# Kernel optimization log

Measured on AMD Instinct MI355X. Metric: run time of the kernel, lower is better.

The kernel has to match this reference:

```python
import jax, jax.numpy as jnp
from jax import lax
import numpy as np

WINDOW_SIZES = (1, 2, 3)


def _proj(x, w1, b1, w2, b2):
    # gated projection: sigmoid(Linear1) * tanh(Linear2)
    return jax.nn.sigmoid(x @ w1.T + b1) * jnp.tanh(x @ w2.T + b2)


def setup_inputs() -> dict:
    key = jax.random.key(0)
    ks = jax.random.split(key, 16)
    V, E, D = 50000, 1024, 1024
    N, La, Lq = 64, 512, 64
    s = 0.02  # weight scale to keep sigmoid/tanh unsaturated
    return {
        "data_q": jax.random.randint(ks[0], (Lq,), 0, V),
        "data_as": jax.random.randint(ks[1], (N, La), 0, V),
        "emb": jax.random.normal(ks[2], (V, E), jnp.float32),
        "w1": jax.random.normal(ks[3], (D, E), jnp.float32) * s,
        "b1": jnp.zeros((D,), jnp.float32),
        "w2": jax.random.normal(ks[4], (D, E), jnp.float32) * s,
        "b2": jnp.zeros((D,), jnp.float32),
        "cw1": jax.random.normal(ks[5], (D, D, 1), jnp.float32) * s,
        "cb1": jnp.zeros((D,), jnp.float32),
        "cw2": jax.random.normal(ks[6], (D, D, 2), jnp.float32) * s,
        "cb2": jnp.zeros((D,), jnp.float32),
        "cw3": jax.random.normal(ks[7], (D, D, 3), jnp.float32) * s,
        "cb3": jnp.zeros((D,), jnp.float32),
        "lin_w": jax.random.normal(ks[8], (D, 3 * D), jnp.float32) * s,
        "lin_b": jnp.zeros((D,), jnp.float32),
        "soft_w": jax.random.normal(ks[9], (1, D), jnp.float32) * s,
        "soft_b": jnp.zeros((1,), jnp.float32),
    }


def reference(data_q, data_as, emb, w1, b1, w2, b2,
              cw1, cb1, cw2, cb2, cw3, cb3, lin_w, lin_b, soft_w, soft_b):
    N, La = data_as.shape
    a_tok = data_as.reshape(-1)                     # [T] concatenated answers
    emb_a = emb[a_tok]                              # [T, E]
    emb_q = emb[data_q]                             # [Lq, E]
    pa = _proj(emb_a, w1, b1, w2, b2)               # [T, D]
    pq = _proj(emb_q, w1, b1, w2, b2)               # [Lq, D]

    # attention: M_r = q @ a^T ; alpha = softmax over question positions
    M = pq @ pa.T                                   # [Lq, T]
    alpha = jax.nn.softmax(M.T, axis=1)             # [T, Lq]
    Y = alpha @ pq                                  # [T, D]
    sim = pa * Y                                    # elementwise compare (mul)

    starts = jnp.arange(N) * La
    x = sim.T[None]                                 # [1, D, T]
    pools = []
    for w, cw, cb in zip(WINDOW_SIZES, (cw1, cw2, cw3), (cb1, cb2, cb3)):
        conv = lax.conv_general_dilated(
            x, cw, (1,), 'VALID',
            dimension_numbers=('NCW', 'OIW', 'NCW'))[0].T + cb  # [T-w+1, D]
        conv = jax.nn.relu(conv)
        # DMax: per-answer max over rows [start_k, start_k + La - w + 1)
        idx = starts[:, None] + jnp.arange(La - w + 1)[None, :]  # [N, La-w+1]
        pools.append(conv[idx].max(axis=1))          # [N, D]

    cat = jnp.concatenate(pools, axis=1)            # [N, 3D]
    h = jnp.tanh(cat @ lin_w.T + lin_b)             # [N, D]
    logits = (h @ soft_w.T + soft_b).reshape(-1)    # [N]
    return jax.nn.log_softmax(logits)
```

## Files before the change

kernel.cpp:

```cpp
#include <hip/hip_runtime.h>

#define DEV __device__ __forceinline__

typedef __bf16 bf16x8 __attribute__((ext_vector_type(8)));
typedef float f32x4 __attribute__((ext_vector_type(4)));
typedef unsigned short u16;
typedef u16 u16x4 __attribute__((ext_vector_type(4)));

constexpr int T_ANS = 32768;
constexpr int LQ    = 64;
constexpr int M_ALL = T_ANS + LQ;
constexpr int M_PAD = 33024;
constexpr int DIM   = 1024;

DEV u16 f2bf(float x) {
  unsigned u = __float_as_uint(x);
  return (u16)((u + 0x7FFFu + ((u >> 16) & 1u)) >> 16);
}
DEV float bf2f(u16 s) { return __uint_as_float(((unsigned)s) << 16); }

DEV void gl2lds16(const void* g, void* l) {
  __builtin_amdgcn_global_load_lds(
      (const __attribute__((address_space(1))) unsigned int*)g,
      (__attribute__((address_space(3))) unsigned int*)l, 16, 0, 0);
}

#define MF(A, B, C) __builtin_amdgcn_mfma_f32_16x16x32_bf16(A, B, C, 0, 0, 0)
#define LFC(P, OFF) (*(const bf16x8*)((P) + (OFF)))


#define STG(G, LT, R0) gl2lds16((G) + (R0) * 2048 + gOff, (LT) + (R0) * 64 + ldOff)

#define S_TILE(AT, BT, BUF)                                                           \
  { const char* ga_ = (AT); const char* gb_ = (BT); char* lb_ = (BUF);                \
    STG(ga_, lb_, 0); STG(ga_, lb_, 128);                                             \
    STG(gb_, lb_ + 16384, 0); STG(gb_, lb_ + 16384, 128); }

#define VMC4 asm volatile("s_waitcnt vmcnt(4)" ::: "memory");
#define VMC0 asm volatile("s_waitcnt vmcnt(0)" ::: "memory");

#define TILEV3(BUF, STAGES, WAIT)                                                     \
  {                                                                                   \
    STAGES                                                                            \
    const char* Ar = (BUF) + rdA;                                                     \
    const char* Br = (BUF) + 16384 + rdB;                                             \
    bf16x8 a0 = LFC(Ar, 0),    a1 = LFC(Ar, 1024), a2 = LFC(Ar, 2048), a3 = LFC(Ar, 3072); \
    bf16x8 a4 = LFC(Ar, 4096), a5 = LFC(Ar, 5120), a6 = LFC(Ar, 6144), a7 = LFC(Ar, 7168); \
    bf16x8 c0 = LFC(Br, 0), c1 = LFC(Br, 1024), c2 = LFC(Br, 2048), c3 = LFC(Br, 3072);    \
    acc[0][0] = MF(a0, c0, acc[0][0]); acc[0][1] = MF(a0, c1, acc[0][1]);             \
    acc[0][2] = MF(a0, c2, acc[0][2]); acc[0][3] = MF(a0, c3, acc[0][3]);             \
    acc[1][0] = MF(a1, c0, acc[1][0]); acc[1][1] = MF(a1, c1, acc[1][1]);             \
    acc[1][2] = MF(a1, c2, acc[1][2]); acc[1][3] = MF(a1, c3, acc[1][3]);             \
    acc[2][0] = MF(a2, c0, acc[2][0]); acc[2][1] = MF(a2, c1, acc[2][1]);             \
    acc[2][2] = MF(a2, c2, acc[2][2]); acc[2][3] = MF(a2, c3, acc[2][3]);             \
    acc[3][0] = MF(a3, c0, acc[3][0]); acc[3][1] = MF(a3, c1, acc[3][1]);             \
    acc[3][2] = MF(a3, c2, acc[3][2]); acc[3][3] = MF(a3, c3, acc[3][3]);             \
    acc[4][0] = MF(a4, c0, acc[4][0]); acc[4][1] = MF(a4, c1, acc[4][1]);             \
    acc[4][2] = MF(a4, c2, acc[4][2]); acc[4][3] = MF(a4, c3, acc[4][3]);             \
    acc[5][0] = MF(a5, c0, acc[5][0]); acc[5][1] = MF(a5, c1, acc[5][1]);             \
    acc[5][2] = MF(a5, c2, acc[5][2]); acc[5][3] = MF(a5, c3, acc[5][3]);             \
    acc[6][0] = MF(a6, c0, acc[6][0]); acc[6][1] = MF(a6, c1, acc[6][1]);             \
    acc[6][2] = MF(a6, c2, acc[6][2]); acc[6][3] = MF(a6, c3, acc[6][3]);             \
    acc[7][0] = MF(a7, c0, acc[7][0]); acc[7][1] = MF(a7, c1, acc[7][1]);             \
    acc[7][2] = MF(a7, c2, acc[7][2]); acc[7][3] = MF(a7, c3, acc[7][3]);             \
    WAIT                                                                              \
    asm volatile("s_barrier" ::: "memory");                                           \
  }

#define GEMM_V3(NT)                                                                   \
  f32x4 acc[8][4] = {};                                                               \
  const int ldOff = tid * 16;                                                         \
  const int gOff = (tid >> 2) * 2048 + (((tid & 3) ^ ((tid >> 2) & 3)) << 4);         \
  const int blk_ = (((lane >> 4) ^ (lane & 3)) << 4);                                 \
  const int rdA = (wm + (lane & 15)) * 64 + blk_;                                     \
  const int rdB = (wn + (lane & 15)) * 64 + blk_;                                     \
  char* b0_ = lds; char* b1_ = lds + 32768; char* b2_ = lds + 65536; char* b3_ = lds + 98304; \
  S_TILE(Ab(0), Bb(0), b0_) S_TILE(Ab(1), Bb(1), b1_)                                 \
  VMC4                                                                                \
  asm volatile("s_barrier" ::: "memory");                                             \
  for (int g = 0; g < (NT) / 4 - 1; ++g) {                                            \
    const int t = 4 * g;                                                              \
    TILEV3(b0_, S_TILE(Ab(t + 2), Bb(t + 2), b2_), VMC4)                              \
    TILEV3(b1_, S_TILE(Ab(t + 3), Bb(t + 3), b3_), VMC4)                              \
    TILEV3(b2_, S_TILE(Ab(t + 4), Bb(t + 4), b0_), VMC4)                              \
    TILEV3(b3_, S_TILE(Ab(t + 5), Bb(t + 5), b1_), VMC4)                              \
  }                                                                                   \
  {                                                                                   \
    const int t = (NT) - 4;                                                           \
    TILEV3(b0_, S_TILE(Ab(t + 2), Bb(t + 2), b2_), VMC4)                              \
    TILEV3(b1_, S_TILE(Ab(t + 3), Bb(t + 3), b3_), VMC4)                              \
    TILEV3(b2_, , VMC0)                                                               \
    TILEV3(b3_, , )                                                                   \
  }


__global__ __launch_bounds__(256)
void prep_all(const float* __restrict__ w1, const float* __restrict__ w2,
              u16* __restrict__ W12,
              const float* __restrict__ lin_w, u16* __restrict__ linb,
              const float* __restrict__ cw1, const float* __restrict__ cw2,
              const float* __restrict__ cw3, u16* __restrict__ cwb,
              float* __restrict__ cat,
              const int* __restrict__ dq, const int* __restrict__ das,
              const float* __restrict__ emb, u16* __restrict__ X) {
  const int b = blockIdx.x, t = threadIdx.x;
  if (b < 8192) {
    int i = b * 256 + t;
    int n2 = i >> 10, k = i & 1023;
    int j = n2 >> 4, m = n2 & 15;
    const float* src = (j & 1) ? w2 : w1;
    W12[i] = f2bf(src[(size_t)((j >> 1) * 16 + m) * 1024 + k]);
  } else if (b < 11264) {
    int i = (b - 8192) * 256 + t;
    float4 v = ((const float4*)lin_w)[i];
    u16x4 o = { f2bf(v.x), f2bf(v.y), f2bf(v.z), f2bf(v.w) };
    ((u16x4*)linb)[i] = o;
  } else if (b < 23552) {
    int rb = b - 11264;
    int W = 1 + (rb >> 12);
    int i = (rb & 4095) * 256 + t;
    const float* src = (W == 1) ? cw1 : (W == 2) ? cw2 : cw3;
    u16* dst = cwb + ((W == 1) ? 0 : (W == 2) ? (size_t)1 * 1048576 : (size_t)3 * 1048576);
#pragma unroll 3
    for (int k = 0; k < 3; ++k)
      if (k < W)
        dst[(size_t)k * 1048576 + i] = f2bf(src[(size_t)i * W + k]);
  } else if (b < 24320) {
    cat[(b - 23552) * 256 + t] = 0.f;
  } else {
    const int row = b - 24320;
    size_t dsto = (size_t)row * DIM + t * 4;
    if (row >= M_ALL) {
      u16x4 z = {0, 0, 0, 0};
      *(u16x4*)(X + dsto) = z;
      return;
    }
    const int tok = (row < T_ANS) ? das[row] : dq[row - T_ANS];
    float4 v = ((const float4*)(emb + (size_t)tok * DIM))[t];
    u16x4 o = { f2bf(v.x), f2bf(v.y), f2bf(v.z), f2bf(v.w) };
    *(u16x4*)(X + dsto) = o;
  }
}

__global__ void transpose_pq(const u16* __restrict__ pa, u16* __restrict__ pqT) {
  int i = blockIdx.x * 256 + threadIdx.x;
  int e = i >> 6, q = i & 63;
  pqT[i] = pa[(size_t)(T_ANS + q) * DIM + e];
}

__global__ void zero_pad_sim(u16* __restrict__ sim) {
  int i = blockIdx.x * 256 + threadIdx.x;
  if (i < 2 * DIM) sim[(size_t)T_ANS * DIM + i] = 0;
}

__global__ void cast_cat(const float* __restrict__ cat, u16* __restrict__ catb) {
  int i = blockIdx.x * 256 + threadIdx.x;
  if (i < 128 * 3072) {
    int row = i / 3072;
    catb[i] = (row < 64) ? f2bf(cat[i]) : (u16)0;
  }
}


__global__ __launch_bounds__(256)
void proj_g(const u16* __restrict__ X, const u16* __restrict__ W12,
            const float* __restrict__ b1, const float* __restrict__ b2,
            u16* __restrict__ pa) {
  __shared__ alignas(16) u16 sA[128 * 32];
  __shared__ alignas(16) u16 sB[128 * 32];
  const int tid = threadIdx.x, lane = tid & 63;
  const int wid = tid >> 6;
  const int wm = (wid >> 1) * 64, wn = (wid & 1) * 64;
  const int wg = ((int)blockIdx.x % 8) * 516 + (int)blockIdx.x / 8;
  const int tm = (wg >> 4) * 128, tn = (wg & 15) * 128;
  f32x4 acc[4][4] = {};
  for (int k0 = 0; k0 < 1024; k0 += 32) {
#pragma unroll
    for (int j = 0; j < 2; ++j) {
      const int f = tid * 16 + j * 4096;
      const int r = f >> 6, cb = f & 63;
      gl2lds16((const char*)X   + (size_t)(tm + r) * 2048 + k0 * 2 + cb, (char*)sA + f);
      gl2lds16((const char*)W12 + (size_t)(tn + r) * 2048 + k0 * 2 + cb, (char*)sB + f);
    }
    __syncthreads();
    const int lr = lane & 15, lk = (lane >> 4) * 8;
    bf16x8 af[4], bf[4];
#pragma unroll
    for (int i = 0; i < 4; ++i) {
      af[i] = *(const bf16x8*)(sA + (wm + i * 16 + lr) * 32 + lk);
      bf[i] = *(const bf16x8*)(sB + (wn + i * 16 + lr) * 32 + lk);
    }
#pragma unroll
    for (int mi = 0; mi < 4; ++mi)
#pragma unroll
      for (int ni = 0; ni < 4; ++ni)
        acc[mi][ni] = MF(af[mi], bf[ni], acc[mi][ni]);
    __syncthreads();
  }
  const int lr = lane & 15, lg = (lane >> 4) * 4;
#pragma unroll
  for (int np = 0; np < 2; ++np) {
    const int col = ((tn + wn) >> 1) + np * 16 + lr;
    const float b1v = b1[col], b2v = b2[col];
#pragma unroll
    for (int mi = 0; mi < 4; ++mi)
#pragma unroll
      for (int r = 0; r < 4; ++r) {
        const int row = tm + wm + mi * 16 + lg + r;
        const float x1 = acc[mi][2 * np][r] + b1v;
        const float x2 = acc[mi][2 * np + 1][r] + b2v;
        const float sg = 1.f / (1.f + __expf(-x1));
        const float th = 2.f / (1.f + __expf(-2.f * x2)) - 1.f;
        pa[(size_t)row * DIM + col] = f2bf(sg * th);
      }
  }
}


template<int W>
__global__ __launch_bounds__(512, 1)
void conv_g(const u16* __restrict__ sim, const u16* __restrict__ Bw,
            const float* __restrict__ cb, float* __restrict__ cat) {
  extern __shared__ char lds[];
  const int tid = threadIdx.x, lane = tid & 63;
  const int wid = tid >> 6;
  const int wm = (wid >> 2) * 128, wn = (wid & 3) * 64;
  const int lr = lane & 15;
  const int wg = ((int)blockIdx.x % 8) * 64 + (int)blockIdx.x / 8;
  const int tm = (wg >> 2) * 256, tn = (wg & 3) * 256;
  const char* Ag = (const char*)sim + (size_t)tm * 2048;
  const char* Bg = (const char*)Bw + (size_t)tn * 2048;
  auto Ab = [&](int t) { return Ag + (t >> 5) * 2048 + ((t & 31) << 6); };
  auto Bb = [&](int t) { return Bg + (size_t)(t >> 5) * 2097152 + ((t & 31) << 6); };

  GEMM_V3(32 * W)

  const int lg = (lane >> 4) * 4;
  const int n = tm >> 9;
#pragma unroll
  for (int ni = 0; ni < 4; ++ni) {
    const int col = tn + wn + ni * 16 + lr;
    const float cbv = cb[col];
    float vmax = 0.f;
#pragma unroll
    for (int mi = 0; mi < 8; ++mi)
#pragma unroll
      for (int r = 0; r < 4; ++r) {
        const int t = tm + wm + mi * 16 + lg + r;
        float v = fmaxf(acc[mi][ni][r] + cbv, 0.f);
        if ((t & 511) > 512 - W) v = 0.f;
        vmax = fmaxf(vmax, v);
      }
    vmax = fmaxf(vmax, __shfl_xor(vmax, 16));
    vmax = fmaxf(vmax, __shfl_xor(vmax, 32));
    if (lane < 16)
      atomicMax((int*)&cat[(size_t)n * 3072 + (W - 1) * 1024 + col], __float_as_int(vmax));
  }
}


__global__ __launch_bounds__(256, 2)
void attn_s(const u16* __restrict__ pa, float* __restrict__ Spart) {
  __shared__ alignas(16) u16 sA[128 * 32];
  __shared__ alignas(16) u16 sB[64 * 32];
  const int tid = threadIdx.x, lane = tid & 63;
  const int tm = blockIdx.x * 128;
  const int kbase = blockIdx.y * 256;
  const int wid = tid >> 6;
  const int wm = (wid >> 1) * 64, wn = (wid & 1) * 32;
  const u16* pq = pa + (size_t)T_ANS * DIM;
  f32x4 acc[4][2] = {};
  for (int k0 = kbase; k0 < kbase + 256; k0 += 32) {
#pragma unroll
    for (int j = 0; j < 2; ++j) {
      const int f = tid * 16 + j * 4096;
      const int r = f >> 6, cb = f & 63;
      gl2lds16((const char*)pa + (size_t)(tm + r) * 2048 + k0 * 2 + cb, (char*)sA + f);
    }
    {
      const int f = tid * 16;
      const int r = f >> 6, cb = f & 63;
      gl2lds16((const char*)pq + (size_t)r * 2048 + k0 * 2 + cb, (char*)sB + f);
    }
    __syncthreads();
    const int lr = lane & 15, lk = (lane >> 4) * 8;
    bf16x8 af[4], bfr[2];
#pragma unroll
    for (int i = 0; i < 4; ++i)
      af[i] = *(const bf16x8*)(sA + (wm + i * 16 + lr) * 32 + lk);
#pragma unroll
    for (int i = 0; i < 2; ++i)
      bfr[i] = *(const bf16x8*)(sB + (wn + i * 16 + lr) * 32 + lk);
#pragma unroll
    for (int mi = 0; mi < 4; ++mi)
#pragma unroll
      for (int ni = 0; ni < 2; ++ni)
        acc[mi][ni] = MF(af[mi], bfr[ni], acc[mi][ni]);
    __syncthreads();
  }
  const int lr = lane & 15, lg = (lane >> 4) * 4;
  float* Sp = Spart + (size_t)blockIdx.y * (T_ANS * 64);
#pragma unroll
  for (int mi = 0; mi < 4; ++mi)
#pragma unroll
    for (int ni = 0; ni < 2; ++ni)
#pragma unroll
      for (int r = 0; r < 4; ++r) {
        const int row = tm + wm + mi * 16 + lg + r;
        const int col = wn + ni * 16 + lr;
        Sp[(size_t)row * 64 + col] = acc[mi][ni][r];
      }
}

__global__ void softmax64(const float* __restrict__ Spart, u16* __restrict__ alpha) {
  const int row = blockIdx.x * 4 + (threadIdx.x >> 6);
  const int lane = threadIdx.x & 63;
  const size_t o = (size_t)row * 64 + lane;
  float v = Spart[o] + Spart[(size_t)1 * T_ANS * 64 + o]
          + Spart[(size_t)2 * T_ANS * 64 + o] + Spart[(size_t)3 * T_ANS * 64 + o];
  float m = v;
#pragma unroll
  for (int o2 = 32; o2 > 0; o2 >>= 1) m = fmaxf(m, __shfl_xor(m, o2));
  const float e = __expf(v - m);
  float s = e;
#pragma unroll
  for (int o2 = 32; o2 > 0; o2 >>= 1) s += __shfl_xor(s, o2);
  alpha[(size_t)row * 64 + lane] = f2bf(e / s);
}


__global__ __launch_bounds__(256, 2)
void attn_y_sim(const u16* __restrict__ alpha, const u16* __restrict__ pqT,
                const u16* __restrict__ pa, u16* __restrict__ sim) {
  __shared__ alignas(16) u16 sA[128 * 32];
  __shared__ alignas(16) u16 sB[128 * 32];
  const int tid = threadIdx.x, lane = tid & 63;
  const int tm = blockIdx.x * 128, tn = blockIdx.y * 128;
  const int wid = tid >> 6;
  const int wm = (wid >> 1) * 64, wn = (wid & 1) * 64;
  f32x4 acc[4][4] = {};
  for (int k0 = 0; k0 < 64; k0 += 32) {
#pragma unroll
    for (int j = 0; j < 2; ++j) {
      const int f = tid * 16 + j * 4096;
      const int r = f >> 6, cb = f & 63;
      gl2lds16((const char*)alpha + (size_t)(tm + r) * 128 + k0 * 2 + cb, (char*)sA + f);
      gl2lds16((const char*)pqT   + (size_t)(tn + r) * 128 + k0 * 2 + cb, (char*)sB + f);
    }
    __syncthreads();
    const int lr = lane & 15, lk = (lane >> 4) * 8;
    bf16x8 af[4], bfr[4];
#pragma unroll
    for (int i = 0; i < 4; ++i) {
      af[i]  = *(const bf16x8*)(sA + (wm + i * 16 + lr) * 32 + lk);
      bfr[i] = *(const bf16x8*)(sB + (wn + i * 16 + lr) * 32 + lk);
    }
#pragma unroll
    for (int mi = 0; mi < 4; ++mi)
#pragma unroll
      for (int ni = 0; ni < 4; ++ni)
        acc[mi][ni] = MF(af[mi], bfr[ni], acc[mi][ni]);
    __syncthreads();
  }
  const int lr = lane & 15, lg = (lane >> 4) * 4;
#pragma unroll
  for (int ni = 0; ni < 4; ++ni) {
    const int col = tn + wn + ni * 16 + lr;
#pragma unroll
    for (int mi = 0; mi < 4; ++mi)
#pragma unroll
      for (int r = 0; r < 4; ++r) {
        const int row = tm + wm + mi * 16 + lg + r;
        const size_t o = (size_t)row * DIM + col;
        sim[o] = f2bf(bf2f(pa[o]) * acc[mi][ni][r]);
      }
  }
}


__global__ __launch_bounds__(256, 2)
void final_h(const u16* __restrict__ catb, const u16* __restrict__ linb,
             const float* __restrict__ lin_b, float* __restrict__ h) {
  __shared__ alignas(16) u16 sA[128 * 32];
  __shared__ alignas(16) u16 sB[128 * 32];
  const int tid = threadIdx.x, lane = tid & 63;
  const int tn = blockIdx.y * 128;
  const int wid = tid >> 6;
  const int wm = (wid >> 1) * 64, wn = (wid & 1) * 64;
  f32x4 acc[4][4] = {};
  for (int k0 = 0; k0 < 3072; k0 += 32) {
#pragma unroll
    for (int j = 0; j < 2; ++j) {
      const int f = tid * 16 + j * 4096;
      const int r = f >> 6, cb = f & 63;
      gl2lds16((const char*)catb + (size_t)r * 6144 + k0 * 2 + cb, (char*)sA + f);
      gl2lds16((const char*)linb + (size_t)(tn + r) * 6144 + k0 * 2 + cb, (char*)sB + f);
    }
    __syncthreads();
    const int lr = lane & 15, lk = (lane >> 4) * 8;
    bf16x8 af[4], bfr[4];
#pragma unroll
    for (int i = 0; i < 4; ++i) {
      af[i]  = *(const bf16x8*)(sA + (wm + i * 16 + lr) * 32 + lk);
      bfr[i] = *(const bf16x8*)(sB + (wn + i * 16 + lr) * 32 + lk);
    }
#pragma unroll
    for (int mi = 0; mi < 4; ++mi)
#pragma unroll
      for (int ni = 0; ni < 4; ++ni)
        acc[mi][ni] = MF(af[mi], bfr[ni], acc[mi][ni]);
    __syncthreads();
  }
  const int lr = lane & 15, lg = (lane >> 4) * 4;
#pragma unroll
  for (int ni = 0; ni < 4; ++ni) {
    const int col = tn + wn + ni * 16 + lr;
    const float bv = lin_b[col];
#pragma unroll
    for (int mi = 0; mi < 4; ++mi)
#pragma unroll
      for (int r = 0; r < 4; ++r) {
        const int row = wm + mi * 16 + lg + r;
        if (row < 64) {
          const float x = acc[mi][ni][r] + bv;
          h[(size_t)row * DIM + col] = 2.f / (1.f + __expf(-2.f * x)) - 1.f;
        }
      }
  }
}

__global__ void final_logits(const float* __restrict__ h, const float* __restrict__ soft_w,
                             const float* __restrict__ soft_b, float* __restrict__ out) {
  __shared__ float part[256];
  const int t = threadIdx.x;
  const int n = t >> 2, q = t & 3;
  float s = 0.f;
  for (int j = q * 256; j < q * 256 + 256; ++j) s += h[(size_t)n * DIM + j] * soft_w[j];
  part[t] = s;
  __syncthreads();
  if (t < 64) {
    float logit = part[t * 4] + part[t * 4 + 1] + part[t * 4 + 2] + part[t * 4 + 3] + soft_b[0];
    float m = logit;
#pragma unroll
    for (int o = 32; o > 0; o >>= 1) m = fmaxf(m, __shfl_xor(m, o));
    float e = __expf(logit - m);
    float ssum = e;
#pragma unroll
    for (int o = 32; o > 0; o >>= 1) ssum += __shfl_xor(ssum, o);
    out[t] = (logit - m) - logf(ssum);
  }
}


extern "C" void kernel_launch(void* const* d_in, const int* in_sizes, int n_in,
                              void* d_out, int out_size, void* d_ws, size_t ws_size,
                              hipStream_t stream) {
  const int*   data_q  = (const int*)d_in[0];
  const int*   data_as = (const int*)d_in[1];
  const float* emb     = (const float*)d_in[2];
  const float* w1      = (const float*)d_in[3];
  const float* b1      = (const float*)d_in[4];
  const float* w2      = (const float*)d_in[5];
  const float* b2      = (const float*)d_in[6];
  const float* cw1     = (const float*)d_in[7];
  const float* cb1     = (const float*)d_in[8];
  const float* cw2     = (const float*)d_in[9];
  const float* cb2     = (const float*)d_in[10];
  const float* cw3     = (const float*)d_in[11];
  const float* cb3     = (const float*)d_in[12];
  const float* lin_w   = (const float*)d_in[13];
  const float* lin_b   = (const float*)d_in[14];
  const float* soft_w  = (const float*)d_in[15];
  const float* soft_b  = (const float*)d_in[16];
  float* out = (float*)d_out;

  hipFuncSetAttribute((const void*)conv_g<1>, hipFuncAttributeMaxDynamicSharedMemorySize, 131072);
  hipFuncSetAttribute((const void*)conv_g<2>, hipFuncAttributeMaxDynamicSharedMemorySize, 131072);
  hipFuncSetAttribute((const void*)conv_g<3>, hipFuncAttributeMaxDynamicSharedMemorySize, 131072);

  u16* X     = (u16*)d_ws;
  u16* pa    = X    + (size_t)M_PAD * DIM;
  u16* W12   = pa   + (size_t)M_PAD * DIM;
  u16* cwb   = W12  + (size_t)2 * 1024 * 1024;
  u16* linb  = cwb  + (size_t)6 * 1024 * 1024;
  u16* pqT   = linb + (size_t)3 * 1024 * 1024;
  u16* alpha = pqT  + 64 * 1024;
  float* cat = (float*)(alpha + (size_t)T_ANS * 64);
  u16* catb  = (u16*)(cat + 64 * 3072);
  float* h   = (float*)(catb + 128 * 3072);
  u16* simb  = X;
  float* Spart = (float*)X;

  prep_all<<<57344, 256, 0, stream>>>(w1, w2, W12, lin_w, linb, cw1, cw2, cw3, cwb,
                                      cat, data_q, data_as, emb, X);

  proj_g<<<4128, 256, 0, stream>>>(X, W12, b1, b2, pa);
  transpose_pq<<<256, 256, 0, stream>>>(pa, pqT);

  attn_s<<<dim3(T_ANS / 128, 4), 256, 0, stream>>>(pa, Spart);
  softmax64<<<T_ANS / 4, 256, 0, stream>>>(Spart, alpha);
  attn_y_sim<<<dim3(T_ANS / 128, 8), 256, 0, stream>>>(alpha, pqT, pa, simb);
  zero_pad_sim<<<8, 256, 0, stream>>>(simb);

  conv_g<1><<<512, 512, 131072, stream>>>(simb, cwb, cb1, cat);
  conv_g<2><<<512, 512, 131072, stream>>>(simb, cwb + (size_t)1 * 1024 * 1024, cb2, cat);
  conv_g<3><<<512, 512, 131072, stream>>>(simb, cwb + (size_t)3 * 1024 * 1024, cb3, cat);

  cast_cat<<<1536, 256, 0, stream>>>(cat, catb);
  final_h<<<dim3(1, 8), 256, 0, stream>>>(catb, linb, lin_b, h);
  final_logits<<<1, 256, 0, stream>>>(h, soft_w, soft_b, out);
}
```

Before: 743.9 us.

## Fuse three conv window GEMMs into one kernel with staged epilogues

Replaces the three per-window conv GEMM launches with a single kernel that runs all 6 K-tap blocks (1+2+3) in one continuous pipelined loop. The pooling epilogue for each window runs and the accumulators are reset at the window boundaries, while the sim A-tile stays L2/cache-resident across windows. This removes two launches and two pipeline fill/drain phases and improves A-operand reuse. In exchange, blocks do serialized work in one longer kernel, and the epilogue stalls in mid-pipeline while prefetched tiles are in flight.

```diff
diff --git a/kernel.cpp b/kernel.cpp
--- a/kernel.cpp
+++ b/kernel.cpp
@@ -67,31 +67,19 @@
     asm volatile("s_barrier" ::: "memory");                                           \
   }
 
-#define GEMM_V3(NT)                                                                   \
-  f32x4 acc[8][4] = {};                                                               \
+#define CORE_BASES                                                                    \
   const int ldOff = tid * 16;                                                         \
   const int gOff = (tid >> 2) * 2048 + (((tid & 3) ^ ((tid >> 2) & 3)) << 4);         \
   const int blk_ = (((lane >> 4) ^ (lane & 3)) << 4);                                 \
   const int rdA = (wm + (lane & 15)) * 64 + blk_;                                     \
   const int rdB = (wn + (lane & 15)) * 64 + blk_;                                     \
-  char* b0_ = lds; char* b1_ = lds + 32768; char* b2_ = lds + 65536; char* b3_ = lds + 98304; \
-  S_TILE(Ab(0), Bb(0), b0_) S_TILE(Ab(1), Bb(1), b1_)                                 \
-  VMC4                                                                                \
-  asm volatile("s_barrier" ::: "memory");                                             \
-  for (int g = 0; g < (NT) / 4 - 1; ++g) {                                            \
-    const int t = 4 * g;                                                              \
-    TILEV3(b0_, S_TILE(Ab(t + 2), Bb(t + 2), b2_), VMC4)                              \
-    TILEV3(b1_, S_TILE(Ab(t + 3), Bb(t + 3), b3_), VMC4)                              \
-    TILEV3(b2_, S_TILE(Ab(t + 4), Bb(t + 4), b0_), VMC4)                              \
-    TILEV3(b3_, S_TILE(Ab(t + 5), Bb(t + 5), b1_), VMC4)                              \
-  }                                                                                   \
-  {                                                                                   \
-    const int t = (NT) - 4;                                                           \
-    TILEV3(b0_, S_TILE(Ab(t + 2), Bb(t + 2), b2_), VMC4)                              \
-    TILEV3(b1_, S_TILE(Ab(t + 3), Bb(t + 3), b3_), VMC4)                              \
-    TILEV3(b2_, , VMC0)                                                               \
-    TILEV3(b3_, , )                                                                   \
-  }
+  char* b0_ = lds; char* b1_ = lds + 32768; char* b2_ = lds + 65536; char* b3_ = lds + 98304;
+
+#define GROUP4(T0)                                                                    \
+    TILEV3(b0_, S_TILE(Ab((T0) + 2), Bb((T0) + 2), b2_), VMC4)                        \
+    TILEV3(b1_, S_TILE(Ab((T0) + 3), Bb((T0) + 3), b3_), VMC4)                        \
+    TILEV3(b2_, S_TILE(Ab((T0) + 4), Bb((T0) + 4), b0_), VMC4)                        \
+    TILEV3(b3_, S_TILE(Ab((T0) + 5), Bb((T0) + 5), b1_), VMC4)
 
 
 __global__ __launch_bounds__(256)
@@ -217,10 +205,10 @@
 }
 
 
-template<int W>
 __global__ __launch_bounds__(512, 1)
-void conv_g(const u16* __restrict__ sim, const u16* __restrict__ Bw,
-            const float* __restrict__ cb, float* __restrict__ cat) {
+void conv_fused(const u16* __restrict__ sim, const u16* __restrict__ cwb,
+                const float* __restrict__ cb1, const float* __restrict__ cb2,
+                const float* __restrict__ cb3, float* __restrict__ cat) {
   extern __shared__ char lds[];
   const int tid = threadIdx.x, lane = tid & 63;
   const int wid = tid >> 6;
@@ -229,33 +217,60 @@
   const int wg = ((int)blockIdx.x % 8) * 64 + (int)blockIdx.x / 8;
   const int tm = (wg >> 2) * 256, tn = (wg & 3) * 256;
   const char* Ag = (const char*)sim + (size_t)tm * 2048;
-  const char* Bg = (const char*)Bw + (size_t)tn * 2048;
-  auto Ab = [&](int t) { return Ag + (t >> 5) * 2048 + ((t & 31) << 6); };
+  const char* Bg = (const char*)cwb + (size_t)tn * 2048;
+  auto Ab = [&](int t) {
+    const int g = t >> 5;
+    const int tap = g - (g > 0) - 2 * (g > 2);
+    return Ag + tap * 2048 + ((t & 31) << 6);
+  };
   auto Bb = [&](int t) { return Bg + (size_t)(t >> 5) * 2097152 + ((t & 31) << 6); };
 
-  GEMM_V3(32 * W)
+  f32x4 acc[8][4] = {};
+  CORE_BASES
 
   const int lg = (lane >> 4) * 4;
   const int n = tm >> 9;
-#pragma unroll
-  for (int ni = 0; ni < 4; ++ni) {
-    const int col = tn + wn + ni * 16 + lr;
-    const float cbv = cb[col];
-    float vmax = 0.f;
-#pragma unroll
-    for (int mi = 0; mi < 8; ++mi)
-#pragma unroll
-      for (int r = 0; r < 4; ++r) {
-        const int t = tm + wm + mi * 16 + lg + r;
-        float v = fmaxf(acc[mi][ni][r] + cbv, 0.f);
-        if ((t & 511) > 512 - W) v = 0.f;
-        vmax = fmaxf(vmax, v);
-      }
-    vmax = fmaxf(vmax, __shfl_xor(vmax, 16));
-    vmax = fmaxf(vmax, __shfl_xor(vmax, 32));
-    if (lane < 16)
-      atomicMax((int*)&cat[(size_t)n * 3072 + (W - 1) * 1024 + col], __float_as_int(vmax));
-  }
+  auto epi = [&](int W, const float* cb, int outoff) {
+#pragma unroll
+    for (int ni = 0; ni < 4; ++ni) {
+      const int col = tn + wn + ni * 16 + lr;
+      const float cbv = cb[col];
+      float vmax = 0.f;
+#pragma unroll
+      for (int mi = 0; mi < 8; ++mi)
+#pragma unroll
+        for (int r = 0; r < 4; ++r) {
+          const int t = tm + wm + mi * 16 + lg + r;
+          float v = fmaxf(acc[mi][ni][r] + cbv, 0.f);
+          if ((t & 511) > 512 - W) v = 0.f;
+          vmax = fmaxf(vmax, v);
+        }
+      vmax = fmaxf(vmax, __shfl_xor(vmax, 16));
+      vmax = fmaxf(vmax, __shfl_xor(vmax, 32));
+      if (lane < 16)
+        atomicMax((int*)&cat[(size_t)n * 3072 + outoff + col], __float_as_int(vmax));
+    }
+#pragma unroll
+    for (int i = 0; i < 8; ++i)
+#pragma unroll
+      for (int j = 0; j < 4; ++j) acc[i][j] = (f32x4){0.f, 0.f, 0.f, 0.f};
+  };
+
+  S_TILE(Ab(0), Bb(0), b0_) S_TILE(Ab(1), Bb(1), b1_)
+  VMC4
+  asm volatile("s_barrier" ::: "memory");
+  for (int g = 0; g < 8; ++g) { GROUP4(4 * g) }
+  epi(1, cb1, 0);
+  for (int g = 8; g < 24; ++g) { GROUP4(4 * g) }
+  epi(2, cb2, 1024);
+  for (int g = 24; g < 47; ++g) { GROUP4(4 * g) }
+  {
+    TILEV3(b0_, S_TILE(Ab(190), Bb(190), b2_), VMC4)
+    TILEV3(b1_, S_TILE(Ab(191), Bb(191), b3_), VMC4)
+    TILEV3(b2_, , VMC0)
+    TILEV3(b3_, , )
+  }
+  epi(3, cb3, 2048);
 }
 
 
@@ -474,9 +489,7 @@
   const float* soft_b  = (const float*)d_in[16];
   float* out = (float*)d_out;
 
-  hipFuncSetAttribute((const void*)conv_g<1>, hipFuncAttributeMaxDynamicSharedMemorySize, 131072);
-  hipFuncSetAttribute((const void*)conv_g<2>, hipFuncAttributeMaxDynamicSharedMemorySize, 131072);
-  hipFuncSetAttribute((const void*)conv_g<3>, hipFuncAttributeMaxDynamicSharedMemorySize, 131072);
+  hipFuncSetAttribute((const void*)conv_fused, hipFuncAttributeMaxDynamicSharedMemorySize, 131072);
 
   u16* X     = (u16*)d_ws;
   u16* pa    = X    + (size_t)M_PAD * DIM;
@@ -502,9 +515,7 @@
   attn_y_sim<<<dim3(T_ANS / 128, 8), 256, 0, stream>>>(alpha, pqT, pa, simb);
   zero_pad_sim<<<8, 256, 0, stream>>>(simb);
 
-  conv_g<1><<<512, 512, 131072, stream>>>(simb, cwb, cb1, cat);
-  conv_g<2><<<512, 512, 131072, stream>>>(simb, cwb + (size_t)1 * 1024 * 1024, cb2, cat);
-  conv_g<3><<<512, 512, 131072, stream>>>(simb, cwb + (size_t)3 * 1024 * 1024, cb3, cat);
+  conv_fused<<<512, 512, 131072, stream>>>(simb, cwb, cb1, cb2, cb3, cat);
 
   cast_cat<<<1536, 256, 0, stream>>>(cat, catb);
   final_h<<<dim3(1, 8), 256, 0, stream>>>(catb, linb, lin_b, h);
```

Measured after the change: 736.6 us. Within noise of the previous version (-1.0%).
